# Optimization experiments

Hardware: AMD Instinct MI355X
Metric: run time of the kernel (lower is better)

Reference implementation:

```python
import jax, jax.numpy as jnp
import numpy as np

B, S, D = 2, 2048, 1024
H, DH = 16, 64
NEG = -1e9


def setup_inputs() -> dict:
    key = jax.random.key(0)
    ks = jax.random.split(key, 4)
    hidden_states = jax.random.normal(ks[0], (B, S, D), dtype=jnp.float32)
    # additive causal mask: 0 where allowed, -1e9 where masked
    causal = jnp.tril(jnp.ones((S, S), dtype=bool))
    attention_mask = jnp.where(causal, 0.0, NEG).astype(jnp.float32)[None, None]
    Wqkv = jax.random.normal(ks[1], (D, 3 * H * DH), dtype=jnp.float32) * (1.0 / np.sqrt(D))
    bqkv = jnp.zeros((3 * H * DH,), dtype=jnp.float32)
    Wproj = jax.random.normal(ks[2], (H * DH, D), dtype=jnp.float32) * (1.0 / np.sqrt(H * DH))
    bproj = jnp.zeros((D,), dtype=jnp.float32)
    return {"hidden_states": hidden_states, "attention_mask": attention_mask,
            "Wqkv": Wqkv, "bqkv": bqkv, "Wproj": Wproj, "bproj": bproj}


def reference(hidden_states, attention_mask, Wqkv, bqkv, Wproj, bproj):
    b, s, _ = hidden_states.shape
    scale = 1.0 / np.sqrt(DH)
    qkv = hidden_states @ Wqkv + bqkv                      # [b, s, 3*H*DH]
    q, k, v = jnp.split(qkv, 3, axis=-1)
    # [b, s, H*DH] -> [b, H, s, DH]
    def split_heads(x):
        return x.reshape(b, s, H, DH).transpose(0, 2, 1, 3)
    q, k, v = split_heads(q), split_heads(k), split_heads(v)
    scores = jnp.einsum('bhqd,bhkd->bhqk', q, k) * scale   # [b, H, s, s]
    scores = scores + attention_mask
    probs = jax.nn.softmax(scores, axis=-1)
    attn = jnp.einsum('bhqk,bhkd->bhqd', probs, v)         # [b, H, s, DH]
    attn = attn.transpose(0, 2, 1, 3).reshape(b, s, H * DH)
    out = attn @ Wproj + bproj                             # [b, s, D]
    return out
```

## Files before the change

### kernel.cpp

```cpp
#include <hip/hip_runtime.h>
#include <stdint.h>

#define B_ 2
#define S_ 2048
#define D_ 1024
#define H_ 16
#define DH_ 64
#define M_ 4096
#define LOG2E 1.44269504088896340736f

typedef __attribute__((ext_vector_type(8))) short short8;
typedef __attribute__((ext_vector_type(4))) float f32x4;

__device__ __forceinline__ unsigned short f2bf(float f) {
  union { float f; uint32_t u; } x; x.f = f;
  uint32_t u = x.u;
  u += 0x7FFFu + ((u >> 16) & 1u);
  return (unsigned short)(u >> 16);
}

__device__ __forceinline__ void gll16(const void* g, void* l) {
  __builtin_amdgcn_global_load_lds(
      (__attribute__((address_space(1))) void*)(g),
      (__attribute__((address_space(3))) void*)(l), 16, 0, 0);
}

__global__ __launch_bounds__(256) void k_cvt(const float* __restrict__ in,
                                             unsigned short* __restrict__ out, int n4) {
  int i = blockIdx.x * 256 + threadIdx.x;
  if (i < n4) {
    float4 v = reinterpret_cast<const float4*>(in)[i];
    ushort4 o;
    o.x = f2bf(v.x); o.y = f2bf(v.y); o.z = f2bf(v.z); o.w = f2bf(v.w);
    reinterpret_cast<ushort4*>(out)[i] = o;
  }
}

__global__ __launch_bounds__(256) void k_cvt_t(const float* __restrict__ W,
                                               unsigned short* __restrict__ WT,
                                               int K, int N) {
  __shared__ unsigned short tile[32][33];
  const int n0 = blockIdx.x * 32, k0 = blockIdx.y * 32;
  const int tx = threadIdx.x & 31, ty = threadIdx.x >> 5;
#pragma unroll
  for (int i = 0; i < 4; i++) {
    int k = ty + i * 8;
    tile[k][tx] = f2bf(W[(long)(k0 + k) * N + n0 + tx]);
  }
  __syncthreads();
#pragma unroll
  for (int i = 0; i < 4; i++) {
    int n = ty + i * 8;
    WT[(long)(n0 + n) * K + k0 + tx] = tile[tx][n];
  }
}

template <int MODE>
__global__ __launch_bounds__(256) void k_gemm(
    const unsigned short* __restrict__ A,
    const unsigned short* __restrict__ BT,
    const float* __restrict__ bias,
    void* __restrict__ out0,
    unsigned short* __restrict__ outk,
    unsigned short* __restrict__ outv,
    int M, int N, int K) {
  __shared__ __align__(16) unsigned short lds_a[128 * 32];
  __shared__ __align__(16) unsigned short lds_b[128 * 32];
  const int t = threadIdx.x;
  const int w = t >> 6, l = t & 63;
  const int g = l >> 4, x = l & 15;
  const int wr = w >> 1, wc = w & 1;
  const long m0 = (long)blockIdx.x * 128, n0 = (long)blockIdx.y * 128;

  f32x4 acc[4][4];
#pragma unroll
  for (int i = 0; i < 4; i++)
#pragma unroll
    for (int j = 0; j < 4; j++) acc[i][j] = (f32x4){0.f, 0.f, 0.f, 0.f};

  const unsigned short* ga = A + (m0 + 16 * w + (l >> 2)) * (long)K + (l & 3) * 8;
  const unsigned short* gb = BT + (n0 + 16 * w + (l >> 2)) * (long)K + (l & 3) * 8;
  unsigned short* la = lds_a + w * 512;
  unsigned short* lb = lds_b + w * 512;

  for (int k0 = 0; k0 < K; k0 += 32) {
    __syncthreads();
    gll16(ga + k0, la);
    gll16(ga + k0 + 64 * (long)K, la + 2048);
    gll16(gb + k0, lb);
    gll16(gb + k0 + 64 * (long)K, lb + 2048);
    __syncthreads();
    short8 af[4], bfr[4];
#pragma unroll
    for (int i = 0; i < 4; i++)
      af[i] = *reinterpret_cast<const short8*>(lds_a + (wr * 64 + i * 16 + x) * 32 + g * 8);
#pragma unroll
    for (int j = 0; j < 4; j++)
      bfr[j] = *reinterpret_cast<const short8*>(lds_b + (wc * 64 + j * 16 + x) * 32 + g * 8);
#pragma unroll
    for (int i = 0; i < 4; i++)
#pragma unroll
      for (int j = 0; j < 4; j++)
        acc[i][j] = __builtin_amdgcn_mfma_f32_16x16x32_bf16(af[i], bfr[j], acc[i][j], 0, 0, 0);
  }

#pragma unroll
  for (int i = 0; i < 4; i++) {
#pragma unroll
    for (int j = 0; j < 4; j++) {
#pragma unroll
      for (int r = 0; r < 4; r++) {
        const long m = m0 + wr * 64 + i * 16 + 4 * g + r;
        const long n = n0 + wc * 64 + j * 16 + x;
        float v = acc[i][j][r] + bias[n];
        if (MODE == 1) {
          ((float*)out0)[m * N + n] = v;
        } else {
          const int b = (int)(m >> 11), s = (int)(m & 2047);
          const int which = (int)(n >> 10);
          const int rem = (int)(n & 1023);
          const int h = rem >> 6, d = rem & 63;
          const long idx = (((long)(b * H_ + h)) * S_ + s) * DH_ + d;
          unsigned short bv = f2bf(v);
          if (which == 0) ((unsigned short*)out0)[idx] = bv;
          else if (which == 1) outk[idx] = bv;
          else outv[idx] = bv;
        }
      }
    }
  }
}

__global__ __launch_bounds__(256) void k_tr_v(const unsigned short* __restrict__ v,
                                              unsigned short* __restrict__ vt) {
  __shared__ __align__(16) unsigned short tile[64][72];
  const int bh = blockIdx.y;
  const int s0 = blockIdx.x * 64;
  const int t = threadIdx.x;
  const int r = t >> 2;
  const int c = (t & 3) * 16;
  const unsigned short* src = v + ((long)bh * S_ + s0 + r) * DH_ + c;
  *reinterpret_cast<short8*>(&tile[r][c]) = *reinterpret_cast<const short8*>(src);
  *reinterpret_cast<short8*>(&tile[r][c + 8]) = *reinterpret_cast<const short8*>(src + 8);
  __syncthreads();
  unsigned short* dst = vt + ((long)bh * DH_ + r) * S_ + s0 + c;
#pragma unroll
  for (int jj = 0; jj < 2; jj++) {
    short8 o;
#pragma unroll
    for (int j = 0; j < 8; j++) o[j] = (short)tile[c + jj * 8 + j][r];
    *reinterpret_cast<short8*>(dst + jj * 8) = o;
  }
}

__global__ __launch_bounds__(256) void k_attn(const unsigned short* __restrict__ qb_,
                                              const unsigned short* __restrict__ kb,
                                              const unsigned short* __restrict__ vt,
                                              unsigned short* __restrict__ attn_out) {
  __shared__ __align__(16) unsigned short lds_k[64 * 64];
  __shared__ __align__(16) unsigned short lds_v[64 * 64];
  __shared__ __align__(16) unsigned short lds_p[4 * 16 * 64];

  const int t = threadIdx.x;
  const int w = t >> 6, l = t & 63;
  const int g = l >> 4, x = l & 15;
  const int lr = l >> 3, lc = l & 7;
  const int sch = lc ^ lr;
  const int bh = blockIdx.y;
  const int b = bh >> 4, h = bh & 15;

  const long kvbase = (long)bh * S_ * DH_;
  unsigned short* pl = lds_p + w * 1024;

#pragma unroll 1
  for (int pass = 0; pass < 2; pass++) {
    const int qtile = pass ? blockIdx.x : (31 - blockIdx.x);
    const int q0 = qtile * 64;

    short8 qf[2];
    {
      const unsigned short* qp = qb_ + kvbase + (long)(q0 + w * 16 + x) * DH_ + g * 8;
      qf[0] = *reinterpret_cast<const short8*>(qp);
      qf[1] = *reinterpret_cast<const short8*>(qp + 32);
    }

    f32x4 oacc[4];
#pragma unroll
    for (int dt = 0; dt < 4; dt++) oacc[dt] = (f32x4){0.f, 0.f, 0.f, 0.f};
    float mrow[4], lrow[4];
#pragma unroll
    for (int r = 0; r < 4; r++) { mrow[r] = -3.0e38f; lrow[r] = 0.f; }

    const int kv_end = q0 + 64;
    for (int kv0 = 0; kv0 < kv_end; kv0 += 64) {
      __syncthreads();
      {
        const unsigned short* ks = kb + kvbase + (long)(kv0 + 8 * w + lr) * DH_ + sch * 8;
        gll16(ks, lds_k + w * 512);
        gll16(ks + 32 * DH_, lds_k + w * 512 + 2048);
        const unsigned short* vs = vt + ((long)bh * DH_ + 8 * w + lr) * S_ + kv0 + sch * 8;
        gll16(vs, lds_v + w * 512);
        gll16(vs + 32 * (long)S_, lds_v + w * 512 + 2048);
      }
      __syncthreads();

      f32x4 sacc[4];
#pragma unroll
      for (int n = 0; n < 4; n++) {
        sacc[n] = (f32x4){0.f, 0.f, 0.f, 0.f};
#pragma unroll
        for (int c = 0; c < 2; c++) {
          short8 kf = *reinterpret_cast<const short8*>(
              lds_k + (n * 16 + x) * 64 + (((4 * c + g) ^ (x & 7)) << 3));
          sacc[n] = __builtin_amdgcn_mfma_f32_16x16x32_bf16(qf[c], kf, sacc[n], 0, 0, 0);
        }
      }

      float mloc[4] = {-3.0e38f, -3.0e38f, -3.0e38f, -3.0e38f};
      const int qgb = q0 + w * 16 + 4 * g;
#pragma unroll
      for (int n = 0; n < 4; n++) {
        const int kvg = kv0 + n * 16 + x;
#pragma unroll
        for (int r = 0; r < 4; r++) {
          float s = sacc[n][r] * 0.125f;
          if (kvg > qgb + r) s = -1.0e9f;
          sacc[n][r] = s;
          mloc[r] = fmaxf(mloc[r], s);
        }
      }
#pragma unroll
      for (int off = 1; off <= 8; off <<= 1)
#pragma unroll
        for (int r = 0; r < 4; r++)
          mloc[r] = fmaxf(mloc[r], __shfl_xor(mloc[r], off, 64));

      float fsc[4], psum[4];
#pragma unroll
      for (int r = 0; r < 4; r++) {
        float mnew = fmaxf(mrow[r], mloc[r]);
        fsc[r] = exp2f((mrow[r] - mnew) * LOG2E);
        mrow[r] = mnew;
        psum[r] = 0.f;
      }
#pragma unroll
      for (int n = 0; n < 4; n++) {
#pragma unroll
        for (int r = 0; r < 4; r++) {
          float p = exp2f((sacc[n][r] - mrow[r]) * LOG2E);
          psum[r] += p;
          const int row = 4 * g + r;
          pl[row * 64 + (((2 * n + (x >> 3)) ^ (row & 7)) << 3) + (x & 7)] = f2bf(p);
        }
      }
#pragma unroll
      for (int off = 1; off <= 8; off <<= 1)
#pragma unroll
        for (int r = 0; r < 4; r++)
          psum[r] += __shfl_xor(psum[r], off, 64);
#pragma unroll
      for (int r = 0; r < 4; r++) lrow[r] = lrow[r] * fsc[r] + psum[r];
#pragma unroll
      for (int dt = 0; dt < 4; dt++)
#pragma unroll
        for (int r = 0; r < 4; r++) oacc[dt][r] *= fsc[r];

#pragma unroll
      for (int c2 = 0; c2 < 2; c2++) {
        short8 pa = *reinterpret_cast<const short8*>(
            pl + x * 64 + (((4 * c2 + g) ^ (x & 7)) << 3));
#pragma unroll
        for (int dt = 0; dt < 4; dt++) {
          short8 vf = *reinterpret_cast<const short8*>(
              lds_v + (dt * 16 + x) * 64 + (((4 * c2 + g) ^ (x & 7)) << 3));
          oacc[dt] = __builtin_amdgcn_mfma_f32_16x16x32_bf16(pa, vf, oacc[dt], 0, 0, 0);
        }
      }
    }

#pragma unroll
    for (int dt = 0; dt < 4; dt++) {
#pragma unroll
      for (int r = 0; r < 4; r++) {
        float o = oacc[dt][r] / lrow[r];
        const long row = (long)b * S_ + q0 + w * 16 + 4 * g + r;
        attn_out[row * (H_ * DH_) + h * DH_ + dt * 16 + x] = f2bf(o);
      }
    }
  }
}

extern "C" void kernel_launch(void* const* d_in, const int* in_sizes, int n_in,
                              void* d_out, int out_size, void* d_ws, size_t ws_size,
                              hipStream_t stream) {
  (void)in_sizes; (void)n_in; (void)out_size; (void)ws_size;
  const float* hs    = (const float*)d_in[0];
  const float* Wqkv  = (const float*)d_in[2];
  const float* bqkv  = (const float*)d_in[3];
  const float* Wproj = (const float*)d_in[4];
  const float* bproj = (const float*)d_in[5];
  float* out = (float*)d_out;

  unsigned short* ws    = (unsigned short*)d_ws;
  unsigned short* hid   = ws;
  unsigned short* wqkvT = hid + 4194304;
  unsigned short* wprT  = wqkvT + 3145728;
  unsigned short* q_b   = wprT + 1048576;
  unsigned short* k_b   = q_b + 4194304;
  unsigned short* v_b   = k_b + 4194304;
  unsigned short* vt_b  = v_b + 4194304;
  unsigned short* ao    = vt_b + 4194304;

  k_cvt<<<4096, 256, 0, stream>>>(hs, hid, 1048576);
  k_cvt_t<<<dim3(96, 32), 256, 0, stream>>>(Wqkv, wqkvT, 1024, 3072);
  k_cvt_t<<<dim3(32, 32), 256, 0, stream>>>(Wproj, wprT, 1024, 1024);
  k_gemm<0><<<dim3(32, 24), 256, 0, stream>>>(hid, wqkvT, bqkv, (void*)q_b, k_b, v_b,
                                              4096, 3072, 1024);
  k_tr_v<<<dim3(32, 32), 256, 0, stream>>>(v_b, vt_b);
  k_attn<<<dim3(16, 32), 256, 0, stream>>>(q_b, k_b, vt_b, ao);
  k_gemm<1><<<dim3(32, 8), 256, 0, stream>>>(ao, wprT, bproj, (void*)out, nullptr, nullptr,
                                             4096, 1024, 1024);
}
```

Measured before the change: 245.3 us.

## Rewrite attention with 32x32 MFMA, transposed scores, double-buffered KV and lazy rescale

The flash-attention kernel now gives each wave 32 query rows and uses 32x32x16 bf16 MFMA. It computes S^T = K·Q^T so that each lane holds one query column, which lets row max and row sum be done mostly in registers. P is repacked for the PV MFMA with cross-half shuffles instead of going through LDS. K and V^T tiles are double-buffered in LDS so the next tile's global loads overlap compute, and there is one barrier per iteration. The running max is only updated when it grows by more than 8 (log2 units), and causal masking is applied only on diagonal tiles. The grid is halved to 128-row query chunks with load-balanced pairing, launched at one block per CU, which lowers occupancy.

Result: faster. 239.4 us (-2.4%).

```diff
diff --git a/kernel.cpp b/kernel.cpp
--- a/kernel.cpp
+++ b/kernel.cpp
@@ -11,12 +11,17 @@
 
 typedef __attribute__((ext_vector_type(8))) short short8;
 typedef __attribute__((ext_vector_type(4))) float f32x4;
+typedef __attribute__((ext_vector_type(16))) float f32x16;
 
 __device__ __forceinline__ unsigned short f2bf(float f) {
   union { float f; uint32_t u; } x; x.f = f;
   uint32_t u = x.u;
   u += 0x7FFFu + ((u >> 16) & 1u);
   return (unsigned short)(u >> 16);
+}
+
+__device__ __forceinline__ unsigned int pack_bf(float lo, float hi2) {
+  return (unsigned int)f2bf(lo) | ((unsigned int)f2bf(hi2) << 16);
 }
 
 __device__ __forceinline__ void gll16(const void* g, void* l) {
@@ -153,139 +158,181 @@
   }
 }
 
-__global__ __launch_bounds__(256) void k_attn(const unsigned short* __restrict__ qb_,
-                                              const unsigned short* __restrict__ kb,
-                                              const unsigned short* __restrict__ vt,
-                                              unsigned short* __restrict__ attn_out) {
-  __shared__ __align__(16) unsigned short lds_k[64 * 64];
-  __shared__ __align__(16) unsigned short lds_v[64 * 64];
-  __shared__ __align__(16) unsigned short lds_p[4 * 16 * 64];
-
-  const int t = threadIdx.x;
-  const int w = t >> 6, l = t & 63;
-  const int g = l >> 4, x = l & 15;
-  const int lr = l >> 3, lc = l & 7;
-  const int sch = lc ^ lr;
+__global__ __launch_bounds__(256, 1) void k_attn(const unsigned short* __restrict__ qb_,
+                                                 const unsigned short* __restrict__ kb,
+                                                 const unsigned short* __restrict__ vt,
+                                                 unsigned short* __restrict__ attn_out) {
+  __shared__ __align__(16) unsigned short lds_k[2][4096];
+  __shared__ __align__(16) unsigned short lds_v[2][4096];
+
+  const int t0 = threadIdx.x;
+  const int w = t0 >> 6, l = t0 & 63;
+  const int q32 = l & 31, hi = l >> 5;
+  const int r7 = q32 & 7;
+  const int lr = l >> 3, sch = (l & 7) ^ lr;
   const int bh = blockIdx.y;
   const int b = bh >> 4, h = bh & 15;
-
   const long kvbase = (long)bh * S_ * DH_;
-  unsigned short* pl = lds_p + w * 1024;
+  const long vtbase = (long)bh * DH_ * S_;
+  const float SC = 0.125f * LOG2E;
 
 #pragma unroll 1
   for (int pass = 0; pass < 2; pass++) {
-    const int qtile = pass ? blockIdx.x : (31 - blockIdx.x);
-    const int q0 = qtile * 64;
-
-    short8 qf[2];
-    {
-      const unsigned short* qp = qb_ + kvbase + (long)(q0 + w * 16 + x) * DH_ + g * 8;
-      qf[0] = *reinterpret_cast<const short8*>(qp);
-      qf[1] = *reinterpret_cast<const short8*>(qp + 32);
+    const int qc = pass ? (15 - blockIdx.x) : blockIdx.x;
+    const int q0p = qc * 128;
+    const int q0w = q0p + 32 * w;
+    const int qg = q0w + q32;
+    const int nt = 2 * qc + 2;
+
+    short8 qf[4];
+#pragma unroll
+    for (int f = 0; f < 4; f++)
+      qf[f] = *reinterpret_cast<const short8*>(qb_ + kvbase + (long)qg * DH_ + 16 * f + 8 * hi);
+
+#pragma unroll
+    for (int i = 0; i < 2; i++) {
+      gll16(kb + kvbase + (long)(16 * w + 8 * i + lr) * DH_ + sch * 8,
+            &lds_k[0][w * 1024 + i * 512]);
+      gll16(vt + vtbase + (long)(16 * w + 8 * i + lr) * S_ + sch * 8,
+            &lds_v[0][w * 1024 + i * 512]);
     }
 
-    f32x4 oacc[4];
-#pragma unroll
-    for (int dt = 0; dt < 4; dt++) oacc[dt] = (f32x4){0.f, 0.f, 0.f, 0.f};
-    float mrow[4], lrow[4];
-#pragma unroll
-    for (int r = 0; r < 4; r++) { mrow[r] = -3.0e38f; lrow[r] = 0.f; }
-
-    const int kv_end = q0 + 64;
-    for (int kv0 = 0; kv0 < kv_end; kv0 += 64) {
+    f32x16 oacc[2];
+#pragma unroll
+    for (int dt = 0; dt < 2; dt++)
+#pragma unroll
+      for (int r = 0; r < 16; r++) oacc[dt][r] = 0.f;
+    float m = -1.0e30f, lown = 0.f;
+
+    asm volatile("s_waitcnt vmcnt(0)" ::: "memory");
+    __syncthreads();
+
+    for (int tt = 0; tt < nt; tt++) {
+      const int kv0 = tt * 64;
+      if (tt + 1 < nt) {
+        const int nb = (tt + 1) & 1;
+        const int kvn = kv0 + 64;
+#pragma unroll
+        for (int i = 0; i < 2; i++) {
+          gll16(kb + kvbase + (long)(kvn + 16 * w + 8 * i + lr) * DH_ + sch * 8,
+                &lds_k[nb][w * 1024 + i * 512]);
+          gll16(vt + vtbase + (long)(16 * w + 8 * i + lr) * S_ + kvn + sch * 8,
+                &lds_v[nb][w * 1024 + i * 512]);
+        }
+      }
+
+      if (kv0 <= q0w + 31) {
+        const unsigned short* lk = lds_k[tt & 1];
+        const unsigned short* lv = lds_v[tt & 1];
+
+        f32x16 sa[2];
+#pragma unroll
+        for (int ks = 0; ks < 2; ks++) {
+#pragma unroll
+          for (int r = 0; r < 16; r++) sa[ks][r] = 0.f;
+#pragma unroll
+          for (int f = 0; f < 4; f++) {
+            short8 kf = *reinterpret_cast<const short8*>(
+                lk + (32 * ks + q32) * 64 + (((2 * f + hi) ^ r7) << 3));
+            sa[ks] = __builtin_amdgcn_mfma_f32_32x32x16_bf16(kf, qf[f], sa[ks], 0, 0, 0);
+          }
+        }
+
+        float p[32];
+#pragma unroll
+        for (int ks = 0; ks < 2; ks++)
+#pragma unroll
+          for (int r = 0; r < 16; r++) p[16 * ks + r] = sa[ks][r] * SC;
+
+        const bool diag = (kv0 + 63 > q0w);
+        if (diag) {
+#pragma unroll
+          for (int ks = 0; ks < 2; ks++)
+#pragma unroll
+            for (int r = 0; r < 16; r++) {
+              const int kvg = kv0 + 32 * ks + (r & 3) + 8 * (r >> 2) + 4 * hi;
+              if (kvg > qg) p[16 * ks + r] = -1.0e30f;
+            }
+        }
+
+        float mx[16];
+#pragma unroll
+        for (int r = 0; r < 16; r++) mx[r] = fmaxf(p[r], p[r + 16]);
+#pragma unroll
+        for (int st = 8; st >= 1; st >>= 1)
+#pragma unroll
+          for (int r = 0; r < 8; r++)
+            if (r < st) mx[r] = fmaxf(mx[r], mx[r + st]);
+        float pmax = fmaxf(mx[0], __shfl_xor(mx[0], 32, 64));
+
+        if (__any(pmax > m + 8.0f)) {
+          const float mn = fmaxf(m, pmax);
+          const float fsc = exp2f(m - mn);
+          m = mn;
+          lown *= fsc;
+#pragma unroll
+          for (int r = 0; r < 16; r++) {
+            const int rr = (r & 3) + 8 * (r >> 2) + 4 * hi;
+            const float fr = __int_as_float(
+                __builtin_amdgcn_ds_bpermute(rr << 2, __float_as_int(fsc)));
+            oacc[0][r] *= fr;
+            oacc[1][r] *= fr;
+          }
+        }
+
+#pragma unroll
+        for (int i = 0; i < 32; i++) p[i] = exp2f(p[i] - m);
+
+        float sm[16];
+#pragma unroll
+        for (int r = 0; r < 16; r++) sm[r] = p[r] + p[r + 16];
+#pragma unroll
+        for (int st = 8; st >= 1; st >>= 1)
+#pragma unroll
+          for (int r = 0; r < 8; r++)
+            if (r < st) sm[r] += sm[r + st];
+        lown += sm[0];
+
+#pragma unroll
+        for (int s4 = 0; s4 < 4; s4++) {
+          const int bse = 8 * s4;
+          unsigned int t0 = pack_bf(p[bse + 0], p[bse + 1]);
+          unsigned int t1 = pack_bf(p[bse + 2], p[bse + 3]);
+          unsigned int t2 = pack_bf(p[bse + 4], p[bse + 5]);
+          unsigned int t3 = pack_bf(p[bse + 6], p[bse + 7]);
+          unsigned int t0x = __shfl_xor(t0, 32, 64);
+          unsigned int t1x = __shfl_xor(t1, 32, 64);
+          unsigned int t2x = __shfl_xor(t2, 32, 64);
+          unsigned int t3x = __shfl_xor(t3, 32, 64);
+          union { unsigned int u[4]; short8 s8; } pa;
+          pa.u[0] = hi ? t2x : t0;
+          pa.u[1] = hi ? t3x : t1;
+          pa.u[2] = hi ? t2 : t0x;
+          pa.u[3] = hi ? t3 : t1x;
+#pragma unroll
+          for (int dt = 0; dt < 2; dt++) {
+            short8 vf = *reinterpret_cast<const short8*>(
+                lv + (32 * dt + q32) * 64 + (((2 * s4 + hi) ^ r7) << 3));
+            oacc[dt] = __builtin_amdgcn_mfma_f32_32x32x16_bf16(pa.s8, vf, oacc[dt], 0, 0, 0);
+          }
+        }
+      }
+
+      asm volatile("s_waitcnt vmcnt(0)" ::: "memory");
       __syncthreads();
-      {
-        const unsigned short* ks = kb + kvbase + (long)(kv0 + 8 * w + lr) * DH_ + sch * 8;
-        gll16(ks, lds_k + w * 512);
-        gll16(ks + 32 * DH_, lds_k + w * 512 + 2048);
-        const unsigned short* vs = vt + ((long)bh * DH_ + 8 * w + lr) * S_ + kv0 + sch * 8;
-        gll16(vs, lds_v + w * 512);
-        gll16(vs + 32 * (long)S_, lds_v + w * 512 + 2048);
-      }
-      __syncthreads();
-
-      f32x4 sacc[4];
-#pragma unroll
-      for (int n = 0; n < 4; n++) {
-        sacc[n] = (f32x4){0.f, 0.f, 0.f, 0.f};
-#pragma unroll
-        for (int c = 0; c < 2; c++) {
-          short8 kf = *reinterpret_cast<const short8*>(
-              lds_k + (n * 16 + x) * 64 + (((4 * c + g) ^ (x & 7)) << 3));
-          sacc[n] = __builtin_amdgcn_mfma_f32_16x16x32_bf16(qf[c], kf, sacc[n], 0, 0, 0);
-        }
-      }
-
-      float mloc[4] = {-3.0e38f, -3.0e38f, -3.0e38f, -3.0e38f};
-      const int qgb = q0 + w * 16 + 4 * g;
-#pragma unroll
-      for (int n = 0; n < 4; n++) {
-        const int kvg = kv0 + n * 16 + x;
-#pragma unroll
-        for (int r = 0; r < 4; r++) {
-          float s = sacc[n][r] * 0.125f;
-          if (kvg > qgb + r) s = -1.0e9f;
-          sacc[n][r] = s;
-          mloc[r] = fmaxf(mloc[r], s);
-        }
-      }
-#pragma unroll
-      for (int off = 1; off <= 8; off <<= 1)
-#pragma unroll
-        for (int r = 0; r < 4; r++)
-          mloc[r] = fmaxf(mloc[r], __shfl_xor(mloc[r], off, 64));
-
-      float fsc[4], psum[4];
-#pragma unroll
-      for (int r = 0; r < 4; r++) {
-        float mnew = fmaxf(mrow[r], mloc[r]);
-        fsc[r] = exp2f((mrow[r] - mnew) * LOG2E);
-        mrow[r] = mnew;
-        psum[r] = 0.f;
-      }
-#pragma unroll
-      for (int n = 0; n < 4; n++) {
-#pragma unroll
-        for (int r = 0; r < 4; r++) {
-          float p = exp2f((sacc[n][r] - mrow[r]) * LOG2E);
-          psum[r] += p;
-          const int row = 4 * g + r;
-          pl[row * 64 + (((2 * n + (x >> 3)) ^ (row & 7)) << 3) + (x & 7)] = f2bf(p);
-        }
-      }
-#pragma unroll
-      for (int off = 1; off <= 8; off <<= 1)
-#pragma unroll
-        for (int r = 0; r < 4; r++)
-          psum[r] += __shfl_xor(psum[r], off, 64);
-#pragma unroll
-      for (int r = 0; r < 4; r++) lrow[r] = lrow[r] * fsc[r] + psum[r];
-#pragma unroll
-      for (int dt = 0; dt < 4; dt++)
-#pragma unroll
-        for (int r = 0; r < 4; r++) oacc[dt][r] *= fsc[r];
-
-#pragma unroll
-      for (int c2 = 0; c2 < 2; c2++) {
-        short8 pa = *reinterpret_cast<const short8*>(
-            pl + x * 64 + (((4 * c2 + g) ^ (x & 7)) << 3));
-#pragma unroll
-        for (int dt = 0; dt < 4; dt++) {
-          short8 vf = *reinterpret_cast<const short8*>(
-              lds_v + (dt * 16 + x) * 64 + (((4 * c2 + g) ^ (x & 7)) << 3));
-          oacc[dt] = __builtin_amdgcn_mfma_f32_16x16x32_bf16(pa, vf, oacc[dt], 0, 0, 0);
-        }
-      }
     }
 
-#pragma unroll
-    for (int dt = 0; dt < 4; dt++) {
-#pragma unroll
-      for (int r = 0; r < 4; r++) {
-        float o = oacc[dt][r] / lrow[r];
-        const long row = (long)b * S_ + q0 + w * 16 + 4 * g + r;
-        attn_out[row * (H_ * DH_) + h * DH_ + dt * 16 + x] = f2bf(o);
-      }
+    const float lt = lown + __shfl_xor(lown, 32, 64);
+    const float linv = 1.0f / lt;
+#pragma unroll
+    for (int r = 0; r < 16; r++) {
+      const int rr = (r & 3) + 8 * (r >> 2) + 4 * hi;
+      const float li = __int_as_float(
+          __builtin_amdgcn_ds_bpermute(rr << 2, __float_as_int(linv)));
+      const long row = (long)b * S_ + q0w + rr;
+#pragma unroll
+      for (int dt = 0; dt < 2; dt++)
+        attn_out[row * (H_ * DH_) + h * DH_ + 32 * dt + q32] = f2bf(oacc[dt][r] * li);
     }
   }
 }
@@ -317,7 +364,7 @@
   k_gemm<0><<<dim3(32, 24), 256, 0, stream>>>(hid, wqkvT, bqkv, (void*)q_b, k_b, v_b,
                                               4096, 3072, 1024);
   k_tr_v<<<dim3(32, 32), 256, 0, stream>>>(v_b, vt_b);
-  k_attn<<<dim3(16, 32), 256, 0, stream>>>(q_b, k_b, vt_b, ao);
+  k_attn<<<dim3(8, 32), 256, 0, stream>>>(q_b, k_b, vt_b, ao);
   k_gemm<1><<<dim3(32, 8), 256, 0, stream>>>(ao, wprT, bproj, (void*)out, nullptr, nullptr,
                                              4096, 1024, 1024);
 }
```
